# Kernel optimization log

Hardware: AMD Instinct MI355X
Metric: run time of the kernel (lower is better)

Reference implementation:

```python
import jax, jax.numpy as jnp
import numpy as np

SPACING = 0.25
CHANNELS = 32
MAX_VAL = 5.0
ENC_FEATS = 128
GRID_N = int(round(2 * MAX_VAL / SPACING)) + 1  # 41
BATCH = 131072

# Uniform cubic B-spline basis matrix: weights(t) = [1, t, t^2, t^3] @ M
CUBIC_B_SPLINE_MATRIX = (1.0 / 6.0) * jnp.array(
    [[1.0, 4.0, 1.0, 0.0],
     [-3.0, 0.0, 3.0, 0.0],
     [3.0, -6.0, 3.0, 0.0],
     [-1.0, 3.0, -3.0, 1.0]], dtype=jnp.float32)


def setup_inputs() -> dict:
    key = jax.random.key(0)
    k1, k2, k3, k4 = jax.random.split(key, 4)
    nb_params = jax.random.normal(k1, (BATCH, 3), dtype=jnp.float32) * 3.0
    lig_grid = jax.random.normal(k2, (CHANNELS, GRID_N, GRID_N, GRID_N), dtype=jnp.float32) * 0.1
    enc_w = jax.random.normal(k3, (ENC_FEATS, CHANNELS), dtype=jnp.float32) / np.sqrt(CHANNELS)
    enc_b = jax.random.normal(k4, (ENC_FEATS,), dtype=jnp.float32) * 0.01
    return {"nb_params": nb_params, "lig_grid": lig_grid, "enc_w": enc_w, "enc_b": enc_b}


def interpolate_grid_3d(grid, coords, interp_matrix):
    # grid: [C, N, N, N]; coords in [0,1]^3: [B, 3]
    N = grid.shape[1]
    u = coords * (N - 1)                       # continuous grid coords [B,3]
    base = jnp.floor(u).astype(jnp.int32)
    t = u - base                               # fractional part [B,3]
    offs = jnp.arange(-1, 3, dtype=jnp.int32)  # 4-point cubic stencil
    idx = jnp.clip(base[:, None, :] + offs[None, :, None], 0, N - 1)  # [B,4,3]
    # per-axis B-spline weights: [B,3,4]
    tp = jnp.stack([jnp.ones_like(t), t, t * t, t * t * t], axis=-1)
    w = jnp.einsum('bdk,kj->bdj', tp, interp_matrix)
    ix, iy, iz = idx[:, :, 0], idx[:, :, 1], idx[:, :, 2]
    # gather 4x4x4 neighborhood: [C,B,4,4,4]
    vals = grid[:, ix[:, :, None, None], iy[:, None, :, None], iz[:, None, None, :]]
    # tricubic weighted sum -> [B,C]
    return jnp.einsum('cbijk,bi,bj,bk->bc', vals, w[:, 0], w[:, 1], w[:, 2])


def reference(nb_params, lig_grid, enc_w, enc_b):
    nb_norm = 0.5 + 0.5 * (nb_params / MAX_VAL)
    nb_norm = jnp.clip(nb_norm, 0.0, 1.0)
    lig_x = interpolate_grid_3d(lig_grid, nb_norm, CUBIC_B_SPLINE_MATRIX)  # [B,C]
    return lig_x @ enc_w.T + enc_b  # [B, ENC_FEATS]
```

## Files before the change

kernel.cpp:

```cpp
#include <hip/hip_runtime.h>
#include <hip/hip_fp16.h>
#include <cstdint>

constexpr int GN   = 41;
constexpr int VOX  = GN * GN * GN;
constexpr int CH   = 32;
constexpr int EF   = 128;
constexpr int TILE = 64;

typedef _Float16 h2 __attribute__((ext_vector_type(2)));
typedef _Float16 h8 __attribute__((ext_vector_type(8)));
typedef float    f4 __attribute__((ext_vector_type(4)));

__device__ __forceinline__ uint32_t pack_h2(float a, float b) {
    __half2 h = __floats2half2_rn(a, b);
    return __builtin_bit_cast(uint32_t, h);
}

__global__ __launch_bounds__(256) void prep_k(
    const float* __restrict__ src, const float* __restrict__ enc_w,
    __half* __restrict__ gT, uint32_t* __restrict__ ewB) {
    int idx = blockIdx.x * 256 + threadIdx.x;
    if (idx < VOX * 4) {
        int s  = idx >> 2;
        int ck = idx & 3;
        float v[8];
#pragma unroll
        for (int i = 0; i < 8; ++i) v[i] = src[(ck * 8 + i) * VOX + s];
        *reinterpret_cast<uint4*>(gT + (size_t)s * CH + ck * 8) =
            make_uint4(pack_h2(v[0], v[1]), pack_h2(v[2], v[3]),
                       pack_h2(v[4], v[5]), pack_h2(v[6], v[7]));
    }
    int pid = idx - VOX * 4;
    if (pid >= 0 && pid < 512) {
        int nt = pid >> 6;
        int l  = pid & 63;
        int f  = nt * 16 + (l & 15);
        int k0 = (l >> 4) * 8;
        const float* wr = enc_w + f * CH + k0;
        float4 a = *reinterpret_cast<const float4*>(wr);
        float4 b = *reinterpret_cast<const float4*>(wr + 4);
        *reinterpret_cast<uint4*>(ewB + (size_t)pid * 4) =
            make_uint4(pack_h2(a.x, a.y), pack_h2(a.z, a.w),
                       pack_h2(b.x, b.y), pack_h2(b.z, b.w));
    }
}

__device__ __forceinline__ void bspline_w(float t, float w[4]) {
    float t2 = t * t, t3 = t2 * t;
    const float k = 1.0f / 6.0f;
    w[0] = k * (1.0f - 3.0f * t + 3.0f * t2 - t3);
    w[1] = k * (4.0f - 6.0f * t2 + 3.0f * t3);
    w[2] = k * (1.0f + 3.0f * t + 3.0f * t2 - 3.0f * t3);
    w[3] = k * t3;
}

__device__ __forceinline__ void fma_mix_lo(float& a, float w, uint32_t p) {
    asm("v_fma_mix_f32 %0, %1, %2, %0 op_sel:[0,0,0] op_sel_hi:[0,1,0]"
        : "+v"(a) : "v"(w), "v"(p));
}
__device__ __forceinline__ void fma_mix_hi(float& a, float w, uint32_t p) {
    asm("v_fma_mix_f32 %0, %1, %2, %0 op_sel:[0,1,0] op_sel_hi:[0,1,0]"
        : "+v"(a) : "v"(w), "v"(p));
}

__global__ __launch_bounds__(256, 3) void lig_main(
    const float* __restrict__ nb, const __half* __restrict__ gT,
    const uint32_t* __restrict__ ewB, const float* __restrict__ enc_b,
    float* __restrict__ out, int batch) {

    __shared__ __align__(16) uint32_t xs[TILE * 16];

    const int tid  = threadIdx.x;
    const int lane = tid & 63;
    const int wv   = tid >> 6;
    const int eq   = lane >> 4;
    const int zsl  = (lane >> 2) & 3;
    const int ck   = (lane & 3) * 8;
    const int base_e = blockIdx.x * TILE;
    (void)batch;

    float q0[4], q1[4], q2[4];
#pragma unroll
    for (int qi = 0; qi < 4; ++qi) {
        const int e = base_e + wv * 16 + qi * 4 + eq;
        q0[qi] = __builtin_nontemporal_load(nb + 3 * e);
        q1[qi] = __builtin_nontemporal_load(nb + 3 * e + 1);
        q2[qi] = __builtin_nontemporal_load(nb + 3 * e + 2);
    }

#pragma unroll
    for (int qi = 0; qi < 4; ++qi) {
        const int eloc = wv * 16 + qi * 4 + eq;

        float ux = fminf(fmaxf(0.5f + 0.1f * q0[qi], 0.0f), 1.0f) * 40.0f;
        float uy = fminf(fmaxf(0.5f + 0.1f * q1[qi], 0.0f), 1.0f) * 40.0f;
        float uz = fminf(fmaxf(0.5f + 0.1f * q2[qi], 0.0f), 1.0f) * 40.0f;
        int bx = (int)ux, by = (int)uy, bz = (int)uz;
        float wx[4], wy[4], wz[4];
        bspline_w(ux - (float)bx, wx);
        bspline_w(uy - (float)by, wy);
        bspline_w(uz - (float)bz, wz);

        const float wzl = wz[zsl];
#pragma unroll
        for (int o = 0; o < 4; ++o) wx[o] *= wzl;

        int X[4], Y[4];
#pragma unroll
        for (int o = 0; o < 4; ++o) {
            X[o] = min(max(bx + o - 1, 0), GN - 1) * (GN * GN * CH);
            Y[o] = min(max(by + o - 1, 0), GN - 1) * (GN * CH);
        }
        const int Zoff = min(max(bz + zsl - 1, 0), GN - 1) * CH + ck;

        uint4 raw[16];
#pragma unroll
        for (int i = 0; i < 4; ++i)
#pragma unroll
            for (int j = 0; j < 4; ++j)
                raw[i * 4 + j] =
                    *reinterpret_cast<const uint4*>(gT + (X[i] + Y[j] + Zoff));

        __builtin_amdgcn_sched_barrier(0);

        float acc[8];
#pragma unroll
        for (int k = 0; k < 8; ++k) acc[k] = 0.0f;

#pragma unroll
        for (int i = 0; i < 4; ++i) {
#pragma unroll
            for (int j = 0; j < 4; ++j) {
                const uint4 r = raw[i * 4 + j];
                const float wt = wx[i] * wy[j];
                fma_mix_lo(acc[0], wt, r.x);
                fma_mix_hi(acc[1], wt, r.x);
                fma_mix_lo(acc[2], wt, r.y);
                fma_mix_hi(acc[3], wt, r.y);
                fma_mix_lo(acc[4], wt, r.z);
                fma_mix_hi(acc[5], wt, r.z);
                fma_mix_lo(acc[6], wt, r.w);
                fma_mix_hi(acc[7], wt, r.w);
            }
        }

#pragma unroll
        for (int k = 0; k < 8; ++k) {
            acc[k] += __shfl_xor(acc[k], 4);
            acc[k] += __shfl_xor(acc[k], 8);
        }

        if ((lane & 12) == 0) {
            uint32_t d0 = __builtin_bit_cast(
                uint32_t, __builtin_amdgcn_cvt_pkrtz(acc[0], acc[1]));
            uint32_t d1 = __builtin_bit_cast(
                uint32_t, __builtin_amdgcn_cvt_pkrtz(acc[2], acc[3]));
            uint32_t d2 = __builtin_bit_cast(
                uint32_t, __builtin_amdgcn_cvt_pkrtz(acc[4], acc[5]));
            uint32_t d3 = __builtin_bit_cast(
                uint32_t, __builtin_amdgcn_cvt_pkrtz(acc[6], acc[7]));
            *reinterpret_cast<uint4*>(&xs[eloc * 16 + (lane & 3) * 4]) =
                make_uint4(d0, d1, d2, d3);
        }
    }

    const int col = lane & 15;
    const int kg  = lane >> 4;

    const h8 af = *reinterpret_cast<const h8*>(
        &xs[(wv * 16 + col) * 16 + kg * 4]);

    float* ob = out + (size_t)(base_e + wv * 16 + kg * 4) * EF + col;

#pragma unroll
    for (int nt = 0; nt < 8; ++nt) {
        const h8 bf = *reinterpret_cast<const h8*>(
            ewB + ((size_t)nt * 64 + lane) * 4);
        const float bias = enc_b[nt * 16 + col];
        f4 acc = {bias, bias, bias, bias};
        acc = __builtin_amdgcn_mfma_f32_16x16x32_f16(af, bf, acc, 0, 0, 0);
#pragma unroll
        for (int r = 0; r < 4; ++r)
            __builtin_nontemporal_store(acc[r],
                                        ob + (size_t)r * EF + nt * 16);
    }
}

extern "C" void kernel_launch(void* const* d_in, const int* in_sizes, int n_in,
                              void* d_out, int out_size, void* d_ws,
                              size_t ws_size, hipStream_t stream) {
    const float* nb   = (const float*)d_in[0];
    const float* grid = (const float*)d_in[1];
    const float* ew   = (const float*)d_in[2];
    const float* eb   = (const float*)d_in[3];
    float*       out  = (float*)d_out;
    __half*      gTh  = (__half*)d_ws;
    uint32_t*    ewB  = (uint32_t*)(gTh + (size_t)VOX * CH);

    int batch = in_sizes[0] / 3;

    int prep_blocks = (VOX * 4 + 512 + 255) / 256;
    prep_k<<<prep_blocks, 256, 0, stream>>>(grid, ew, gTh, ewB);
    lig_main<<<batch / TILE, 256, 0, stream>>>(nb, gTh, ewB, eb, out, batch);
}
```

Measured before the change: 118.9 us.

## Double-buffer gather windows to overlap loads with FMA across query iterations

Replaces the sequential per-query gather-then-accumulate loop with a two-deep software pipeline: the gathers for the next query are issued before the current query's accumulation, using two 16-register raw buffers. The aim is to hide global gather latency within a wave instead of relying on other waves. To make room for the doubled register footprint, the occupancy hint drops from 3 to 2 blocks per CU, which trades wave-level latency hiding for instruction-level overlap.

```diff
diff --git a/kernel.cpp b/kernel.cpp
--- a/kernel.cpp
+++ b/kernel.cpp
@@ -64,7 +64,64 @@
         : "+v"(a) : "v"(w), "v"(p));
 }
 
-__global__ __launch_bounds__(256, 3) void lig_main(
+#define WIN_ISSUE(QI, RAW, WX, WY)                                           \
+    {                                                                        \
+        float ux = fminf(fmaxf(0.5f + 0.1f * q0[QI], 0.0f), 1.0f) * 40.0f;   \
+        float uy = fminf(fmaxf(0.5f + 0.1f * q1[QI], 0.0f), 1.0f) * 40.0f;   \
+        float uz = fminf(fmaxf(0.5f + 0.1f * q2[QI], 0.0f), 1.0f) * 40.0f;   \
+        int bx = (int)ux, by = (int)uy, bz = (int)uz;                        \
+        float wz_[4];                                                        \
+        bspline_w(ux - (float)bx, WX);                                       \
+        bspline_w(uy - (float)by, WY);                                       \
+        bspline_w(uz - (float)bz, wz_);                                      \
+        const float wzl = wz_[zsl];                                          \
+        _Pragma("unroll") for (int o = 0; o < 4; ++o) WX[o] *= wzl;          \
+        int X_[4], Y_[4];                                                    \
+        _Pragma("unroll") for (int o = 0; o < 4; ++o) {                      \
+            X_[o] = min(max(bx + o - 1, 0), GN - 1) * (GN * GN * CH);        \
+            Y_[o] = min(max(by + o - 1, 0), GN - 1) * (GN * CH);             \
+        }                                                                    \
+        const int Zo = min(max(bz + zsl - 1, 0), GN - 1) * CH + ck;          \
+        _Pragma("unroll") for (int i = 0; i < 4; ++i)                        \
+            _Pragma("unroll") for (int j = 0; j < 4; ++j)                    \
+                RAW[i * 4 + j] = *reinterpret_cast<const uint4*>(            \
+                    gT + (X_[i] + Y_[j] + Zo));                              \
+    }
+
+#define WIN_CONSUME(QI, RAW, WX, WY)                                         \
+    {                                                                        \
+        const int eloc = wv * 16 + (QI) * 4 + eq;                            \
+        float acc[8];                                                        \
+        _Pragma("unroll") for (int k = 0; k < 8; ++k) acc[k] = 0.0f;         \
+        _Pragma("unroll") for (int i = 0; i < 4; ++i) {                      \
+            _Pragma("unroll") for (int j = 0; j < 4; ++j) {                  \
+                const uint4 r = RAW[i * 4 + j];                              \
+                const float wt = WX[i] * WY[j];                              \
+                fma_mix_lo(acc[0], wt, r.x); fma_mix_hi(acc[1], wt, r.x);    \
+                fma_mix_lo(acc[2], wt, r.y); fma_mix_hi(acc[3], wt, r.y);    \
+                fma_mix_lo(acc[4], wt, r.z); fma_mix_hi(acc[5], wt, r.z);    \
+                fma_mix_lo(acc[6], wt, r.w); fma_mix_hi(acc[7], wt, r.w);    \
+            }                                                                \
+        }                                                                    \
+        _Pragma("unroll") for (int k = 0; k < 8; ++k) {                      \
+            acc[k] += __shfl_xor(acc[k], 4);                                 \
+            acc[k] += __shfl_xor(acc[k], 8);                                 \
+        }                                                                    \
+        if ((lane & 12) == 0) {                                              \
+            uint32_t d0 = __builtin_bit_cast(                                \
+                uint32_t, __builtin_amdgcn_cvt_pkrtz(acc[0], acc[1]));       \
+            uint32_t d1 = __builtin_bit_cast(                                \
+                uint32_t, __builtin_amdgcn_cvt_pkrtz(acc[2], acc[3]));       \
+            uint32_t d2 = __builtin_bit_cast(                                \
+                uint32_t, __builtin_amdgcn_cvt_pkrtz(acc[4], acc[5]));       \
+            uint32_t d3 = __builtin_bit_cast(                                \
+                uint32_t, __builtin_amdgcn_cvt_pkrtz(acc[6], acc[7]));       \
+            *reinterpret_cast<uint4*>(&xs[eloc * 16 + (lane & 3) * 4]) =     \
+                make_uint4(d0, d1, d2, d3);                                  \
+        }                                                                    \
+    }
+
+__global__ __launch_bounds__(256, 2) void lig_main(
     const float* __restrict__ nb, const __half* __restrict__ gT,
     const uint32_t* __restrict__ ewB, const float* __restrict__ enc_b,
     float* __restrict__ out, int batch) {
@@ -89,81 +146,23 @@
         q2[qi] = __builtin_nontemporal_load(nb + 3 * e + 2);
     }
 
-#pragma unroll
-    for (int qi = 0; qi < 4; ++qi) {
-        const int eloc = wv * 16 + qi * 4 + eq;
-
-        float ux = fminf(fmaxf(0.5f + 0.1f * q0[qi], 0.0f), 1.0f) * 40.0f;
-        float uy = fminf(fmaxf(0.5f + 0.1f * q1[qi], 0.0f), 1.0f) * 40.0f;
-        float uz = fminf(fmaxf(0.5f + 0.1f * q2[qi], 0.0f), 1.0f) * 40.0f;
-        int bx = (int)ux, by = (int)uy, bz = (int)uz;
-        float wx[4], wy[4], wz[4];
-        bspline_w(ux - (float)bx, wx);
-        bspline_w(uy - (float)by, wy);
-        bspline_w(uz - (float)bz, wz);
-
-        const float wzl = wz[zsl];
-#pragma unroll
-        for (int o = 0; o < 4; ++o) wx[o] *= wzl;
-
-        int X[4], Y[4];
-#pragma unroll
-        for (int o = 0; o < 4; ++o) {
-            X[o] = min(max(bx + o - 1, 0), GN - 1) * (GN * GN * CH);
-            Y[o] = min(max(by + o - 1, 0), GN - 1) * (GN * CH);
-        }
-        const int Zoff = min(max(bz + zsl - 1, 0), GN - 1) * CH + ck;
-
-        uint4 raw[16];
-#pragma unroll
-        for (int i = 0; i < 4; ++i)
-#pragma unroll
-            for (int j = 0; j < 4; ++j)
-                raw[i * 4 + j] =
-                    *reinterpret_cast<const uint4*>(gT + (X[i] + Y[j] + Zoff));
-
-        __builtin_amdgcn_sched_barrier(0);
-
-        float acc[8];
-#pragma unroll
-        for (int k = 0; k < 8; ++k) acc[k] = 0.0f;
-
-#pragma unroll
-        for (int i = 0; i < 4; ++i) {
-#pragma unroll
-            for (int j = 0; j < 4; ++j) {
-                const uint4 r = raw[i * 4 + j];
-                const float wt = wx[i] * wy[j];
-                fma_mix_lo(acc[0], wt, r.x);
-                fma_mix_hi(acc[1], wt, r.x);
-                fma_mix_lo(acc[2], wt, r.y);
-                fma_mix_hi(acc[3], wt, r.y);
-                fma_mix_lo(acc[4], wt, r.z);
-                fma_mix_hi(acc[5], wt, r.z);
-                fma_mix_lo(acc[6], wt, r.w);
-                fma_mix_hi(acc[7], wt, r.w);
-            }
-        }
-
-#pragma unroll
-        for (int k = 0; k < 8; ++k) {
-            acc[k] += __shfl_xor(acc[k], 4);
-            acc[k] += __shfl_xor(acc[k], 8);
-        }
-
-        if ((lane & 12) == 0) {
-            uint32_t d0 = __builtin_bit_cast(
-                uint32_t, __builtin_amdgcn_cvt_pkrtz(acc[0], acc[1]));
-            uint32_t d1 = __builtin_bit_cast(
-                uint32_t, __builtin_amdgcn_cvt_pkrtz(acc[2], acc[3]));
-            uint32_t d2 = __builtin_bit_cast(
-                uint32_t, __builtin_amdgcn_cvt_pkrtz(acc[4], acc[5]));
-            uint32_t d3 = __builtin_bit_cast(
-                uint32_t, __builtin_amdgcn_cvt_pkrtz(acc[6], acc[7]));
-            *reinterpret_cast<uint4*>(&xs[eloc * 16 + (lane & 3) * 4]) =
-                make_uint4(d0, d1, d2, d3);
-        }
-    }
+    uint4 rA[16], rB[16];
+    float wxA[4], wyA[4], wxB[4], wyB[4];
+
+    WIN_ISSUE(0, rA, wxA, wyA);
+    WIN_ISSUE(1, rB, wxB, wyB);
+    __builtin_amdgcn_sched_barrier(0);
+
+    WIN_CONSUME(0, rA, wxA, wyA);
+    WIN_ISSUE(2, rA, wxA, wyA);
+    __builtin_amdgcn_sched_barrier(0);
+
+    WIN_CONSUME(1, rB, wxB, wyB);
+    WIN_ISSUE(3, rB, wxB, wyB);
+    __builtin_amdgcn_sched_barrier(0);
+
+    WIN_CONSUME(2, rA, wxA, wyA);
+    WIN_CONSUME(3, rB, wxB, wyB);
 
     const int col = lane & 15;
     const int kg  = lane >> 4;
```

New measurement: 120.1 us. Within noise of the previous version (+1.0%).
